# Kernel optimization log

Measured on AMD Instinct MI355X. Metric: run time of the kernel, lower is better.

## Reference

```python
import jax, jax.numpy as jnp
import numpy as np

B, T, D, H = 2, 2048, 512, 8
HD = D // H


def _mha(x, Wi, bi, Wo, bo):
    # torch nn.MultiheadAttention with q=k=v=x, eval mode (no dropout), batch-first math
    b, t, d = x.shape
    qkv = x @ Wi.T + bi                      # (b,t,3D)
    q, k, v = jnp.split(qkv, 3, axis=-1)
    q = q.reshape(b, t, H, HD)
    k = k.reshape(b, t, H, HD)
    v = v.reshape(b, t, H, HD)
    scores = jnp.einsum('bqhd,bkhd->bhqk', q, k) / jnp.sqrt(jnp.float32(HD))
    attn = jax.nn.softmax(scores, axis=-1)   # (b,H,t,t)
    out = jnp.einsum('bhqk,bkhd->bqhd', attn, v).reshape(b, t, d) @ Wo.T + bo
    return out, attn.mean(axis=1)            # weights averaged over heads, torch default


def _block_ids(t, c):
    # importance score is the constant c at every position (grad of sum == ones)
    cum = jnp.cumsum(jnp.full((t,), c, dtype=jnp.float32))
    frac = cum % 1.0
    boundary = (frac < jnp.roll(frac, 1)).astype(jnp.int32)
    return jnp.cumsum(boundary)              # ids in [0, max_blocks]


def _merge(x, ids, m):
    # segment-mean over dynamic blocks; block id 0 (pre-first-boundary) is dropped, as in torch loop i=1..max
    xm = jnp.moveaxis(x, 1, 0)               # (t,b,d)
    sums = jax.ops.segment_sum(xm, ids, num_segments=m + 1)[1:]              # (m,b,d)
    counts = jax.ops.segment_sum(jnp.ones(ids.shape[0], jnp.float32), ids, num_segments=m + 1)[1:]
    merged = sums / (counts[:, None, None] + 1e-10)
    return jnp.moveaxis(merged, 0, 1), counts


def setup_inputs():
    key = jax.random.key(0)
    ks = jax.random.split(key, 12)
    s = 0.02
    d = {'x': jax.random.normal(ks[0], (B, T, D), jnp.float32)}
    for i, n in enumerate(['char', 'block', 'glob']):
        d[n + '_Wi'] = jax.random.normal(ks[1 + 3 * i], (3 * D, D), jnp.float32) * s
        d[n + '_bi'] = jnp.zeros((3 * D,), jnp.float32)
        d[n + '_Wo'] = jax.random.normal(ks[2 + 3 * i], (D, D), jnp.float32) * s
        d[n + '_bo'] = jnp.zeros((D,), jnp.float32)
    d['merge_w'] = jax.random.normal(ks[10], (D,), jnp.float32) * 0.01
    d['merge_b'] = jnp.array([0.37], jnp.float32)
    d['gmerge_w'] = jax.random.normal(ks[11], (D,), jnp.float32) * 0.01
    d['gmerge_b'] = jnp.array([0.41], jnp.float32)
    return d


def reference(x, char_Wi, char_bi, char_Wo, char_bo, block_Wi, block_bi, block_Wo, block_bo,
              glob_Wi, glob_bi, glob_Wo, glob_bo, merge_w, merge_b, gmerge_w, gmerge_b):
    char_out, char_w = _mha(x, char_Wi, char_bi, char_Wo, char_bo)
    c1 = merge_w.sum() + merge_b[0]
    ids1 = _block_ids(T, c1)
    m1 = int(ids1.max())                      # data-independent given weights; concrete in eager
    blocks, cnt1 = _merge(char_out, ids1, m1)
    block_out, block_w = _mha(blocks, block_Wi, block_bi, block_Wo, block_bo)
    c2 = gmerge_w.sum() + gmerge_b[0]
    ids2 = _block_ids(m1, c2)
    m2 = int(ids2.max())
    glob, cnt2 = _merge(block_out, ids2, m2)
    glob_out, glob_w = _mha(glob, glob_Wi, glob_bi, glob_Wo, glob_bo)
    # double repeat_interleave expansion == gather: token t -> char block -> global block
    ids1n = np.asarray(ids1)
    ids2n = np.asarray(ids2)
    token_g = np.where(ids1n >= 1, ids2n[np.maximum(ids1n - 1, 0)], 0)
    tok_idx = np.nonzero(token_g >= 1)[0]
    expanded = glob_out[:, jnp.asarray(token_g[tok_idx] - 1), :]
    return expanded, char_w, block_w, glob_w
```

## Files before the change

### kernel.cpp

```cpp
#include <hip/hip_runtime.h>
#include <cstdint>
#include <cstddef>


#define TB 2
#define TT 2048
#define TD 512
#define TH 8
#define THD 64
#define KC 4

#define MI_M1 0
#define MI_M2 1
#define MI_NTOK 2
#define MI_OFF_CW 3
#define MI_OFF_BW 4
#define MI_OFF_GW 5
#define MI_MCHAR 6
#define MI_MBLOCK 7
#define MI_MGLOB 8
#define MI_SEQC 9
#define MI_SEQB 10
#define MI_SEQG 11

typedef _Float16 half8 __attribute__((ext_vector_type(8)));
typedef _Float16 half4 __attribute__((ext_vector_type(4)));
typedef _Float16 half2_t __attribute__((ext_vector_type(2)));
typedef float floatx4 __attribute__((ext_vector_type(4)));

__device__ __forceinline__ floatx4 mfma16(half8 a, half8 b, floatx4 c) {
  return __builtin_amdgcn_mfma_f32_16x16x32_f16(a, b, c, 0, 0, 0);
}
__device__ __forceinline__ floatx4 mfma16k16(half4 a, half4 b, floatx4 c) {
  return __builtin_amdgcn_mfma_f32_16x16x16f16(a, b, c, 0, 0, 0);
}

__device__ __forceinline__ double fracd(double x) { return x - floor(x); }

__device__ int scan_phase(int n, double c, int* __restrict__ ids,
                          int* __restrict__ startg, float* __restrict__ cntg,
                          int* __restrict__ wsum, int t)
{
  int loc[8];
  const int base = t * 8;
#pragma unroll
  for (int j = 0; j < 8; ++j) {
    const int i = base + j;
    int f = 0;
    if (i < n) {
      const int pidx = (i == 0) ? n : i;
      f = (fracd((double)(i + 1) * c) < fracd((double)pidx * c)) ? 1 : 0;
    }
    loc[j] = f + ((j > 0) ? loc[j - 1] : 0);
  }
  wsum[t] = loc[7];
  __syncthreads();
  for (int off = 1; off < 256; off <<= 1) {
    int u = 0;
    if (t >= off) u = wsum[t - off];
    __syncthreads();
    wsum[t] += u;
    __syncthreads();
  }
  const int excl = wsum[t] - loc[7];
  const int m = wsum[255];
#pragma unroll
  for (int j = 0; j < 8; ++j) {
    const int i = base + j;
    if (i < n) {
      const int id = excl + loc[j];
      ids[i] = id;
      const int f = loc[j] - ((j > 0) ? loc[j - 1] : 0);
      if (f) startg[id - 1] = i;
    }
  }
  __syncthreads();
  for (int j = t; j < m; j += 256)
    cntg[j] = (float)((((j + 1) < m) ? startg[j + 1] : n) - startg[j]);
  __syncthreads();
  return m;
}

__global__ __launch_bounds__(256)
void meta_kernel(const float* __restrict__ mw, const float* __restrict__ mb,
                 const float* __restrict__ gw, const float* __restrict__ gb,
                 int* __restrict__ mi,
                 int* __restrict__ start1, float* __restrict__ cnt1,
                 int* __restrict__ start2, float* __restrict__ cnt2,
                 int* __restrict__ gmap)
{
  __shared__ int ids1[TT];
  __shared__ int ids2[TT];
  __shared__ int wsum[256];
  __shared__ double dsh[256];
  const int t = threadIdx.x;

  double s1 = 0.0, s2 = 0.0;
  for (int i = t; i < TD; i += 256) { s1 += (double)mw[i]; s2 += (double)gw[i]; }
  dsh[t] = s1; __syncthreads();
  for (int off = 128; off > 0; off >>= 1) {
    if (t < off) dsh[t] += dsh[t + off];
    __syncthreads();
  }
  const double c1 = dsh[0] + (double)mb[0];
  __syncthreads();
  dsh[t] = s2; __syncthreads();
  for (int off = 128; off > 0; off >>= 1) {
    if (t < off) dsh[t] += dsh[t + off];
    __syncthreads();
  }
  const double c2 = dsh[0] + (double)gb[0];
  __syncthreads();

  const int m1 = scan_phase(TT, c1, ids1, start1, cnt1, wsum, t);
  const int m2 = scan_phase(m1, c2, ids2, start2, cnt2, wsum, t);

  int i0 = TT;
  if (m1 >= 1 && m2 >= 1) i0 = start1[start2[0]];
  const int ntok = TT - i0;

  if (t == 0) {
    mi[MI_M1] = m1; mi[MI_M2] = m2; mi[MI_NTOK] = ntok;
    const int offcw = TB * ntok * TD;
    mi[MI_OFF_CW] = offcw;
    mi[MI_OFF_BW] = offcw + TB * TT * TT;
    mi[MI_OFF_GW] = offcw + TB * TT * TT + TB * m1 * m1;
    mi[MI_MCHAR] = TB * TT;
    mi[MI_MBLOCK] = TB * m1;
    mi[MI_MGLOB] = TB * m2;
    mi[MI_SEQC] = TT;
    mi[MI_SEQB] = m1;
    mi[MI_SEQG] = m2;
  }
  for (int i = i0 + t; i < TT; i += 256)
    gmap[i - i0] = ids2[ids1[i] - 1] - 1;
}

template <typename OutT, bool SPLIT>
__global__ __launch_bounds__(256)
void gemm_mfma(const float* __restrict__ A, const float* __restrict__ W,
               const float* __restrict__ bias, OutT* __restrict__ C,
               const int* __restrict__ mi, int m_slot, int N)
{
  const int M = mi[m_slot];
  const int bm = blockIdx.y * 128;
  if (bm >= M) return;
  const int bn = blockIdx.x * 64;
  __shared__ _Float16 Ah[128][40];
  __shared__ _Float16 Wh[64][40];
  __shared__ _Float16 Al[SPLIT ? 128 : 1][40];
  __shared__ _Float16 Wl[SPLIT ? 64 : 1][40];

  const int t = threadIdx.x;
  const int wv = t >> 6;
  const int lane = t & 63;
  const int l15 = lane & 15;
  const int quad = lane >> 4;
  const int srowA = t >> 1;
  const int ssegA = (t & 1) * 16;
  const int srowW = t >> 2;
  const int ssegW = (t & 3) * 8;

  floatx4 acc[2][4];
#pragma unroll
  for (int i = 0; i < 2; ++i)
#pragma unroll
    for (int j = 0; j < 4; ++j) acc[i][j] = (floatx4){0.f, 0.f, 0.f, 0.f};

  for (int kk = 0; kk < TD; kk += 32) {
    __syncthreads();
    {
      const int ar = bm + srowA;
#pragma unroll
      for (int u = 0; u < 4; ++u) {
        float4 av = make_float4(0.f, 0.f, 0.f, 0.f);
        if (ar < M) av = *(const float4*)&A[(size_t)ar * TD + kk + ssegA + u * 4];
        const float aa[4] = {av.x, av.y, av.z, av.w};
        half4 hi, lo;
#pragma unroll
        for (int e = 0; e < 4; ++e) {
          const _Float16 h = (_Float16)aa[e];
          hi[e] = h;
          if constexpr (SPLIT) lo[e] = (_Float16)(aa[e] - (float)h);
        }
        *(half4*)&Ah[srowA][ssegA + u * 4] = hi;
        if constexpr (SPLIT) *(half4*)&Al[srowA][ssegA + u * 4] = lo;
      }
#pragma unroll
      for (int u = 0; u < 2; ++u) {
        const float4 wvv = *(const float4*)&W[(size_t)(bn + srowW) * TD + kk + ssegW + u * 4];
        const float ww[4] = {wvv.x, wvv.y, wvv.z, wvv.w};
        half4 hi, lo;
#pragma unroll
        for (int e = 0; e < 4; ++e) {
          const _Float16 h = (_Float16)ww[e];
          hi[e] = h;
          if constexpr (SPLIT) lo[e] = (_Float16)(ww[e] - (float)h);
        }
        *(half4*)&Wh[srowW][ssegW + u * 4] = hi;
        if constexpr (SPLIT) *(half4*)&Wl[srowW][ssegW + u * 4] = lo;
      }
    }
    __syncthreads();
    half8 ah[2], al[2];
#pragma unroll
    for (int mp = 0; mp < 2; ++mp) {
      ah[mp] = *(const half8*)&Ah[wv * 32 + mp * 16 + l15][quad * 8];
      if constexpr (SPLIT) al[mp] = *(const half8*)&Al[wv * 32 + mp * 16 + l15][quad * 8];
    }
#pragma unroll
    for (int np = 0; np < 4; ++np) {
      const half8 bh = *(const half8*)&Wh[np * 16 + l15][quad * 8];
      if constexpr (SPLIT) {
        const half8 bl = *(const half8*)&Wl[np * 16 + l15][quad * 8];
#pragma unroll
        for (int mp = 0; mp < 2; ++mp) {
          acc[mp][np] = mfma16(al[mp], bh, acc[mp][np]);
          acc[mp][np] = mfma16(ah[mp], bl, acc[mp][np]);
          acc[mp][np] = mfma16(ah[mp], bh, acc[mp][np]);
        }
      } else {
#pragma unroll
        for (int mp = 0; mp < 2; ++mp)
          acc[mp][np] = mfma16(ah[mp], bh, acc[mp][np]);
      }
    }
  }
  float bv[4];
#pragma unroll
  for (int np = 0; np < 4; ++np) bv[np] = bias[bn + np * 16 + l15];
#pragma unroll
  for (int mp = 0; mp < 2; ++mp) {
#pragma unroll
    for (int r = 0; r < 4; ++r) {
      const int row = bm + wv * 32 + mp * 16 + quad * 4 + r;
      if (row < M) {
        OutT* cp = &C[(size_t)row * N + bn];
#pragma unroll
        for (int np = 0; np < 4; ++np)
          cp[np * 16 + l15] = (OutT)(acc[mp][np][r] + bv[np]);
      }
    }
  }
}

__global__ __launch_bounds__(256)
void gemm_norm_mfma(const _Float16* __restrict__ Ob, const float* __restrict__ lb,
                    const float* __restrict__ W, const float* __restrict__ bias,
                    float* __restrict__ C, const int* __restrict__ mi,
                    int m_slot, int seq_slot)
{
  const int M = mi[m_slot];
  const int bm = blockIdx.y * 64;
  if (bm >= M) return;
  const int seq = mi[seq_slot];
  const int bn = blockIdx.x * 64;
  __shared__ _Float16 Ah[64][40];
  __shared__ _Float16 Al[64][40];
  __shared__ _Float16 Wh[64][40];
  __shared__ _Float16 Wl[64][40];

  const int t = threadIdx.x;
  const int wv = t >> 6;
  const int lane = t & 63;
  const int l15 = lane & 15;
  const int quad = lane >> 4;
  const int srow = t >> 2;
  const int sseg = (t & 3) * 8;

  const int ar = bm + srow;
  const int ab = (ar >= seq) ? 1 : 0;
  const int aq = ar - ab * seq;

  floatx4 acc[4];
#pragma unroll
  for (int j = 0; j < 4; ++j) acc[j] = (floatx4){0.f, 0.f, 0.f, 0.f};

  for (int kk = 0; kk < TD; kk += 32) {
    __syncthreads();
    {
      float aa[8] = {0.f, 0.f, 0.f, 0.f, 0.f, 0.f, 0.f, 0.f};
      if (ar < M) {
        const size_t off = (size_t)ar * TD + kk + sseg;
#pragma unroll
        for (int z = 0; z < KC; ++z) {
          const half8 hv = *(const half8*)&Ob[(size_t)z * 2097152 + off];
#pragma unroll
          for (int e = 0; e < 8; ++e) aa[e] += (float)hv[e];
        }
        const int h = kk >> 6;
        const size_t lidx = ((size_t)(ab * TH + h)) * 2048 + aq;
        float lt = 0.f;
#pragma unroll
        for (int z = 0; z < KC; ++z) lt += lb[(size_t)z * 32768 + lidx];
        const float linv = 1.f / lt;
#pragma unroll
        for (int e = 0; e < 8; ++e) aa[e] *= linv;
      }
      half8 hi, lo;
#pragma unroll
      for (int e = 0; e < 8; ++e) {
        const _Float16 h = (_Float16)aa[e];
        hi[e] = h; lo[e] = (_Float16)(aa[e] - (float)h);
      }
      *(half8*)&Ah[srow][sseg] = hi;
      *(half8*)&Al[srow][sseg] = lo;

      const float4 w0 = *(const float4*)&W[(size_t)(bn + srow) * TD + kk + sseg];
      const float4 w1 = *(const float4*)&W[(size_t)(bn + srow) * TD + kk + sseg + 4];
      const float ww[8] = {w0.x, w0.y, w0.z, w0.w, w1.x, w1.y, w1.z, w1.w};
      half8 whi, wlo;
#pragma unroll
      for (int e = 0; e < 8; ++e) {
        const _Float16 h = (_Float16)ww[e];
        whi[e] = h; wlo[e] = (_Float16)(ww[e] - (float)h);
      }
      *(half8*)&Wh[srow][sseg] = whi;
      *(half8*)&Wl[srow][sseg] = wlo;
    }
    __syncthreads();
    const half8 ah = *(const half8*)&Ah[wv * 16 + l15][quad * 8];
    const half8 al = *(const half8*)&Al[wv * 16 + l15][quad * 8];
#pragma unroll
    for (int np = 0; np < 4; ++np) {
      const half8 bh = *(const half8*)&Wh[np * 16 + l15][quad * 8];
      const half8 bl = *(const half8*)&Wl[np * 16 + l15][quad * 8];
      acc[np] = mfma16(al, bh, acc[np]);
      acc[np] = mfma16(ah, bl, acc[np]);
      acc[np] = mfma16(ah, bh, acc[np]);
    }
  }
  float bv[4];
#pragma unroll
  for (int np = 0; np < 4; ++np) bv[np] = bias[bn + np * 16 + l15];
#pragma unroll
  for (int r = 0; r < 4; ++r) {
    const int row = bm + wv * 16 + quad * 4 + r;
    if (row < M) {
      float* cp = &C[(size_t)row * 512 + bn];
#pragma unroll
      for (int np = 0; np < 4; ++np)
        cp[np * 16 + l15] = acc[np][r] + bv[np];
    }
  }
}

__global__ __launch_bounds__(256)
void attn1_mfma(const _Float16* __restrict__ qkv,
                float* __restrict__ lbase, _Float16* __restrict__ Obase,
                const int* __restrict__ mi, int seq_slot)
{
  const int seq = mi[seq_slot];
  const int q0 = blockIdx.x * 128;
  if (q0 >= seq) return;
  const int b = blockIdx.y >> 3, h = blockIdx.y & 7;
  const int z = blockIdx.z;
  float* lP = lbase + (size_t)z * 32768;
  _Float16* oP = Obase + (size_t)z * 2097152;
  const int t = threadIdx.x;
  const int wv = t >> 6;
  const int lane = t & 63;
  const int l15 = lane & 15;
  const int quad = lane >> 4;

  __shared__ __align__(16) char smem_raw[18432];
  _Float16 (*Kf)[72] = (_Float16 (*)[72])smem_raw;
  _Float16 (*Vt)[72] = (_Float16 (*)[72])(smem_raw + 9216);
  float    (*Ot)[68] = (float (*)[68])smem_raw;

  half8 qB[2][2];
#pragma unroll
  for (int mp = 0; mp < 2; ++mp) {
    const int qrow = q0 + wv * 32 + mp * 16 + l15;
#pragma unroll
    for (int c = 0; c < 2; ++c) {
      half8 v = {};
      if (qrow < seq)
        v = *(const half8*)&qkv[((size_t)(b * seq + qrow)) * 1536 + h * 64 + c * 32 + quad * 8];
      qB[mp][c] = v;
    }
  }
  half4 onesA;
#pragma unroll
  for (int j = 0; j < 4; ++j) onesA[j] = (_Float16)1.0f;

  floatx4 oacc[2][4];
#pragma unroll
  for (int i = 0; i < 2; ++i)
#pragma unroll
    for (int j = 0; j < 4; ++j) oacc[i][j] = (floatx4){0.f, 0.f, 0.f, 0.f};
  floatx4 lacc[2] = {(floatx4){0.f, 0.f, 0.f, 0.f}, (floatx4){0.f, 0.f, 0.f, 0.f}};

  const int nkt = (seq + 63) >> 6;
  const int nkc = (nkt + KC - 1) / KC;
  const int kt_beg = z * nkc;
  const int kt_end = min(kt_beg + nkc, nkt);

  for (int kt = kt_beg; kt < kt_end; ++kt) {
    const int k0 = kt * 64;
    __syncthreads();
    {
      const int row = t >> 2;
      const int seg = (t & 3) * 16;
      const int kg = k0 + row;
      half8 v0 = {}, v1 = {};
      if (kg < seq) {
        const _Float16* base = &qkv[((size_t)(b * seq + kg)) * 1536 + 512 + h * 64 + seg];
        v0 = *(const half8*)base;
        v1 = *(const half8*)(base + 8);
      }
      *(half8*)&Kf[row][seg] = v0;
      *(half8*)&Kf[row][seg + 8] = v1;
    }
    {
      const int tp = lane & 31;
      const int dsel = lane >> 5;
      const int dbase = wv * 16 + dsel * 8;
      const int kg0 = k0 + tp * 2;
      half8 vA = {}, vB = {};
      if (kg0 < seq)
        vA = *(const half8*)&qkv[((size_t)(b * seq + kg0)) * 1536 + 1024 + h * 64 + dbase];
      if (kg0 + 1 < seq)
        vB = *(const half8*)&qkv[((size_t)(b * seq + kg0 + 1)) * 1536 + 1024 + h * 64 + dbase];
#pragma unroll
      for (int j = 0; j < 8; ++j) {
        half2_t pk; pk[0] = vA[j]; pk[1] = vB[j];
        *(half2_t*)&Vt[dbase + j][tp * 2] = pk;
      }
    }
    __syncthreads();

#pragma unroll
    for (int p = 0; p < 4; ++p) {
      floatx4 sT[2] = {(floatx4){0.f, 0.f, 0.f, 0.f}, (floatx4){0.f, 0.f, 0.f, 0.f}};
#pragma unroll
      for (int c = 0; c < 2; ++c) {
        const half8 kA = *(const half8*)&Kf[p * 16 + l15][c * 32 + quad * 8];
#pragma unroll
        for (int mp = 0; mp < 2; ++mp)
          sT[mp] = mfma16(kA, qB[mp][c], sT[mp]);
      }
      half4 vA[4];
#pragma unroll
      for (int dblk = 0; dblk < 4; ++dblk)
        vA[dblk] = *(const half4*)&Vt[dblk * 16 + l15][p * 16 + quad * 4];
      const int kg = k0 + p * 16 + quad * 4;
#pragma unroll
      for (int mp = 0; mp < 2; ++mp) {
        half4 eB;
#pragma unroll
        for (int r = 0; r < 4; ++r) {
          const float e = (kg + r < seq) ? __expf(sT[mp][r] * 0.125f) : 0.f;
          eB[r] = (_Float16)e;
        }
        lacc[mp] = mfma16k16(onesA, eB, lacc[mp]);
#pragma unroll
        for (int dblk = 0; dblk < 4; ++dblk)
          oacc[mp][dblk] = mfma16k16(vA[dblk], eB, oacc[mp][dblk]);
      }
    }
  }

  __syncthreads();

#pragma unroll
  for (int mp = 0; mp < 2; ++mp) {
#pragma unroll
    for (int dblk = 0; dblk < 4; ++dblk)
      *(floatx4*)&Ot[wv * 16 + l15][dblk * 16 + quad * 4] = oacc[mp][dblk];
    const int ql = lane >> 2;
    const int dseg = (lane & 3) * 4;
    const int qg = q0 + wv * 32 + mp * 16 + ql;
    if (qg < seq) {
      _Float16* op = &oP[((size_t)(b * seq + qg)) * 512 + h * 64];
#pragma unroll
      for (int u = 0; u < 4; ++u) {
        const float4 v = *(const float4*)&Ot[wv * 16 + ql][u * 16 + dseg];
        half4 hv;
        hv[0] = (_Float16)v.x; hv[1] = (_Float16)v.y;
        hv[2] = (_Float16)v.z; hv[3] = (_Float16)v.w;
        *(half4*)(op + u * 16 + dseg) = hv;
      }
    }
    if (quad == 0) {
      const int qg2 = q0 + wv * 32 + mp * 16 + l15;
      if (qg2 < seq)
        lP[((size_t)(b * TH + h)) * 2048 + qg2] = lacc[mp][0];
    }
  }
}

__global__ __launch_bounds__(256)
void attn2_mfma(const _Float16* __restrict__ qkv,
                const float* __restrict__ lb,
                float* __restrict__ outb, const int* __restrict__ mi,
                int seq_slot, int off_slot)
{
  const int seq = mi[seq_slot];
  const int q0 = blockIdx.y * 64;
  const int k0 = blockIdx.x * 128;
  if (q0 >= seq || k0 >= seq) return;
  const int b = blockIdx.z;
  const int woff = mi[off_slot];
  float* wout = outb + (size_t)woff + (size_t)b * seq * seq;

  __shared__ _Float16 Qs[64][72];
  __shared__ _Float16 Ksh[128][72];
  __shared__ float Linv[64];

  const int t = threadIdx.x;
  const int wv = t >> 6;
  const int lane = t & 63;
  const int l15 = lane & 15;
  const int quad = lane >> 4;
  const int srowQ = t >> 2;
  const int ssegQ = (t & 3) * 16;
  const int srowK = t >> 1;
  const int ssegK = (t & 1) * 32;

  floatx4 acc[8];
#pragma unroll
  for (int j = 0; j < 8; ++j) acc[j] = (floatx4){0.f, 0.f, 0.f, 0.f};

  for (int h = 0; h < TH; ++h) {
    __syncthreads();
    {
      const int qr = q0 + srowQ;
      half8 q0v = {}, q1v = {};
      if (qr < seq) {
        const _Float16* base = &qkv[((size_t)(b * seq + qr)) * 1536 + h * 64 + ssegQ];
        q0v = *(const half8*)base;
        q1v = *(const half8*)(base + 8);
      }
      *(half8*)&Qs[srowQ][ssegQ] = q0v;
      *(half8*)&Qs[srowQ][ssegQ + 8] = q1v;

      const int kr = k0 + srowK;
#pragma unroll
      for (int u = 0; u < 4; ++u) {
        half8 kv = {};
        if (kr < seq)
          kv = *(const half8*)&qkv[((size_t)(b * seq + kr)) * 1536 + 512 + h * 64 + ssegK + u * 8];
        *(half8*)&Ksh[srowK][ssegK + u * 8] = kv;
      }
      if (t < 64) {
        float lv = 1.f;
        if (q0 + t < seq) {
          const size_t lidx = ((size_t)(b * TH + h)) * 2048 + q0 + t;
          float lt = 0.f;
#pragma unroll
          for (int z = 0; z < KC; ++z) lt += lb[(size_t)z * 32768 + lidx];
          lv = lt;
        }
        Linv[t] = 1.f / lv;
      }
    }
    __syncthreads();

    half8 af[2];
#pragma unroll
    for (int c = 0; c < 2; ++c)
      af[c] = *(const half8*)&Qs[wv * 16 + l15][c * 32 + quad * 8];
    float lv[4];
#pragma unroll
    for (int r = 0; r < 4; ++r)
      lv[r] = Linv[wv * 16 + quad * 4 + r];

#pragma unroll
    for (int np = 0; np < 8; ++np) {
      half8 bf[2];
#pragma unroll
      for (int c = 0; c < 2; ++c)
        bf[c] = *(const half8*)&Ksh[np * 16 + l15][c * 32 + quad * 8];
      floatx4 s = (floatx4){0.f, 0.f, 0.f, 0.f};
      s = mfma16(af[0], bf[0], s);
      s = mfma16(af[1], bf[1], s);
#pragma unroll
      for (int r = 0; r < 4; ++r)
        acc[np][r] += __expf(s[r] * 0.125f) * lv[r];
    }
  }

#pragma unroll
  for (int r = 0; r < 4; ++r) {
    const int qg = q0 + wv * 16 + quad * 4 + r;
    if (qg >= seq) continue;
    float* rowp = wout + (size_t)qg * seq;
#pragma unroll
    for (int np = 0; np < 8; ++np) {
      const int col = k0 + np * 16 + l15;
      if (col < seq) rowp[col] = acc[np][r] * 0.125f;
    }
  }
}

__global__ __launch_bounds__(256)
void merge_kernel(const float* __restrict__ src, float* __restrict__ dst,
                  const int* __restrict__ start, const float* __restrict__ cnt,
                  const int* __restrict__ mi, int seqin_slot, int seqout_slot)
{
  const int j = blockIdx.x;
  const int b = blockIdx.y;
  const int seqo = mi[seqout_slot];
  if (j >= seqo) return;
  const int seqi = mi[seqin_slot];
  const int s = start[j];
  const float cf = cnt[j];
  const int n = (int)cf;
  const int d0 = threadIdx.x * 2;
  float s0 = 0.f, s1 = 0.f;
  const float* p = &src[((size_t)b * seqi + s) * TD + d0];
  for (int i = 0; i < n; ++i) {
    const float2 v = *(const float2*)p;
    s0 += v.x; s1 += v.y;
    p += TD;
  }
  const float inv = 1.f / (cf + 1e-10f);
  float2 o; o.x = s0 * inv; o.y = s1 * inv;
  *(float2*)&dst[((size_t)b * seqo + j) * TD + d0] = o;
}

__global__ __launch_bounds__(256)
void expand_kernel(const float* __restrict__ gout, float* __restrict__ dout,
                   const int* __restrict__ gmap, const int* __restrict__ mi)
{
  const int j = blockIdx.x;
  const int b = blockIdx.y;
  const int ntok = mi[MI_NTOK];
  if (j >= ntok) return;
  const int m2 = mi[MI_M2];
  const int g = gmap[j];
  const int d0 = threadIdx.x * 2;
  const float2 v = *(const float2*)&gout[((size_t)b * m2 + g) * TD + d0];
  *(float2*)&dout[((size_t)b * ntok + j) * TD + d0] = v;
}

extern "C" void kernel_launch(void* const* d_in, const int* in_sizes, int n_in,
                              void* d_out, int out_size, void* d_ws, size_t ws_size,
                              hipStream_t stream)
{
  const float* x   = (const float*)d_in[0];
  const float* cWi = (const float*)d_in[1];
  const float* cbi = (const float*)d_in[2];
  const float* cWo = (const float*)d_in[3];
  const float* cbo = (const float*)d_in[4];
  const float* bWi = (const float*)d_in[5];
  const float* bbi = (const float*)d_in[6];
  const float* bWo = (const float*)d_in[7];
  const float* bbo = (const float*)d_in[8];
  const float* gWi = (const float*)d_in[9];
  const float* gbi = (const float*)d_in[10];
  const float* gWo = (const float*)d_in[11];
  const float* gbo = (const float*)d_in[12];
  const float* mw  = (const float*)d_in[13];
  const float* mbv = (const float*)d_in[14];
  const float* gw  = (const float*)d_in[15];
  const float* gbv = (const float*)d_in[16];
  float* outf = (float*)d_out;

  char* wsb = (char*)d_ws;
  int*   mi     = (int*)(wsb);
  int*   start1 = (int*)(wsb + 1024);
  float* cnt1   = (float*)(wsb + 1024 + 8192);
  int*   start2 = (int*)(wsb + 1024 + 2 * 8192);
  float* cnt2   = (float*)(wsb + 1024 + 3 * 8192);
  int*   gmap   = (int*)(wsb + 1024 + 4 * 8192);
  float* lbase  = (float*)(wsb + 65536);
  _Float16* qkv = (_Float16*)(wsb + 655360);
  _Float16* Obase = (_Float16*)(wsb + 655360 + 12582912);
  float* stg_o  = (float*)(wsb + 655360 + 12582912 + (size_t)KC * 4194304);
  float* stg_m  = stg_o + 2097152;

  const dim3 blk(256);

  meta_kernel<<<dim3(1), blk, 0, stream>>>(mw, mbv, gw, gbv, mi, start1, cnt1, start2, cnt2, gmap);

  gemm_mfma<_Float16, false><<<dim3(24, 32), blk, 0, stream>>>(x, cWi, cbi, qkv, mi, MI_MCHAR, 1536);
  attn1_mfma<<<dim3(16, 16, KC), blk, 0, stream>>>(qkv, lbase, Obase, mi, MI_SEQC);
  attn2_mfma<<<dim3(16, 32, 2), blk, 0, stream>>>(qkv, lbase, outf, mi, MI_SEQC, MI_OFF_CW);
  gemm_norm_mfma<<<dim3(8, 64), blk, 0, stream>>>(Obase, lbase, cWo, cbo, stg_o, mi, MI_MCHAR, MI_SEQC);
  merge_kernel<<<dim3(2048, 2), blk, 0, stream>>>(stg_o, stg_m, start1, cnt1, mi, MI_SEQC, MI_SEQB);

  gemm_mfma<_Float16, false><<<dim3(24, 32), blk, 0, stream>>>(stg_m, bWi, bbi, qkv, mi, MI_MBLOCK, 1536);
  attn1_mfma<<<dim3(16, 16, KC), blk, 0, stream>>>(qkv, lbase, Obase, mi, MI_SEQB);
  attn2_mfma<<<dim3(16, 32, 2), blk, 0, stream>>>(qkv, lbase, outf, mi, MI_SEQB, MI_OFF_BW);
  gemm_norm_mfma<<<dim3(8, 64), blk, 0, stream>>>(Obase, lbase, bWo, bbo, stg_o, mi, MI_MBLOCK, MI_SEQB);
  merge_kernel<<<dim3(2048, 2), blk, 0, stream>>>(stg_o, stg_m, start2, cnt2, mi, MI_SEQB, MI_SEQG);

  gemm_mfma<_Float16, false><<<dim3(24, 32), blk, 0, stream>>>(stg_m, gWi, gbi, qkv, mi, MI_MGLOB, 1536);
  attn1_mfma<<<dim3(16, 16, KC), blk, 0, stream>>>(qkv, lbase, Obase, mi, MI_SEQG);
  attn2_mfma<<<dim3(16, 32, 2), blk, 0, stream>>>(qkv, lbase, outf, mi, MI_SEQG, MI_OFF_GW);
  gemm_norm_mfma<<<dim3(8, 64), blk, 0, stream>>>(Obase, lbase, gWo, gbo, stg_o, mi, MI_MGLOB, MI_SEQG);
  expand_kernel<<<dim3(2048, 2), blk, 0, stream>>>(stg_o, outf, gmap, mi);

  (void)in_sizes; (void)n_in; (void)out_size; (void)ws_size;
}
```

Baseline: 398.4 us.

## Enlarge attention-weight tile to 128 queries and use exp2 with folded scale

The head-averaged attention-weight kernel now handles 128 query rows per block instead of 64. Each wave computes two 16-row sub-tiles that share the loaded K fragments, and the grid is halved, so K tiles are reloaded from global memory half as often. The exponentials in both attention kernels switch from __expf with a 0.125 scale to exp2f with the scale and log2(e) folded into one constant. The first attention kernel also skips the per-element bounds check on full key tiles. The larger tile doubles accumulator registers and shared memory per block, which may reduce occupancy, and halves the number of blocks.

```diff
diff --git a/kernel.cpp b/kernel.cpp
--- a/kernel.cpp
+++ b/kernel.cpp
@@ -23,6 +23,8 @@
 #define MI_SEQB 10
 #define MI_SEQG 11
 
+#define CEXP 0.1803368801111244f
+
 typedef _Float16 half8 __attribute__((ext_vector_type(8)));
 typedef _Float16 half4 __attribute__((ext_vector_type(4)));
 typedef _Float16 half2_t __attribute__((ext_vector_type(2)));
@@ -398,6 +400,7 @@
 
   for (int kt = kt_beg; kt < kt_end; ++kt) {
     const int k0 = kt * 64;
+    const bool full = (k0 + 64 <= seq);
     __syncthreads();
     {
       const int row = t >> 2;
@@ -448,10 +451,16 @@
 #pragma unroll
       for (int mp = 0; mp < 2; ++mp) {
         half4 eB;
-#pragma unroll
-        for (int r = 0; r < 4; ++r) {
-          const float e = (kg + r < seq) ? __expf(sT[mp][r] * 0.125f) : 0.f;
-          eB[r] = (_Float16)e;
+        if (full) {
+#pragma unroll
+          for (int r = 0; r < 4; ++r)
+            eB[r] = (_Float16)exp2f(sT[mp][r] * CEXP);
+        } else {
+#pragma unroll
+          for (int r = 0; r < 4; ++r) {
+            const float e = (kg + r < seq) ? exp2f(sT[mp][r] * CEXP) : 0.f;
+            eB[r] = (_Float16)e;
+          }
         }
         lacc[mp] = mfma16k16(onesA, eB, lacc[mp]);
 #pragma unroll
@@ -497,53 +506,47 @@
                 int seq_slot, int off_slot)
 {
   const int seq = mi[seq_slot];
-  const int q0 = blockIdx.y * 64;
+  const int q0 = blockIdx.y * 128;
   const int k0 = blockIdx.x * 128;
   if (q0 >= seq || k0 >= seq) return;
   const int b = blockIdx.z;
   const int woff = mi[off_slot];
   float* wout = outb + (size_t)woff + (size_t)b * seq * seq;
 
-  __shared__ _Float16 Qs[64][72];
+  __shared__ _Float16 Qs[128][72];
   __shared__ _Float16 Ksh[128][72];
-  __shared__ float Linv[64];
+  __shared__ float Linv[128];
 
   const int t = threadIdx.x;
   const int wv = t >> 6;
   const int lane = t & 63;
   const int l15 = lane & 15;
   const int quad = lane >> 4;
-  const int srowQ = t >> 2;
-  const int ssegQ = (t & 3) * 16;
-  const int srowK = t >> 1;
-  const int ssegK = (t & 1) * 32;
-
-  floatx4 acc[8];
-#pragma unroll
-  for (int j = 0; j < 8; ++j) acc[j] = (floatx4){0.f, 0.f, 0.f, 0.f};
+  const int srow = t >> 1;
+  const int sseg = (t & 1) * 32;
+
+  floatx4 acc[2][8];
+#pragma unroll
+  for (int i = 0; i < 2; ++i)
+#pragma unroll
+    for (int j = 0; j < 8; ++j) acc[i][j] = (floatx4){0.f, 0.f, 0.f, 0.f};
 
   for (int h = 0; h < TH; ++h) {
     __syncthreads();
     {
-      const int qr = q0 + srowQ;
-      half8 q0v = {}, q1v = {};
-      if (qr < seq) {
-        const _Float16* base = &qkv[((size_t)(b * seq + qr)) * 1536 + h * 64 + ssegQ];
-        q0v = *(const half8*)base;
-        q1v = *(const half8*)(base + 8);
-      }
-      *(half8*)&Qs[srowQ][ssegQ] = q0v;
-      *(half8*)&Qs[srowQ][ssegQ + 8] = q1v;
-
-      const int kr = k0 + srowK;
+      const int qr = q0 + srow;
+      const int kr = k0 + srow;
 #pragma unroll
       for (int u = 0; u < 4; ++u) {
-        half8 kv = {};
+        half8 qv = {}, kv = {};
+        if (qr < seq)
+          qv = *(const half8*)&qkv[((size_t)(b * seq + qr)) * 1536 + h * 64 + sseg + u * 8];
         if (kr < seq)
-          kv = *(const half8*)&qkv[((size_t)(b * seq + kr)) * 1536 + 512 + h * 64 + ssegK + u * 8];
-        *(half8*)&Ksh[srowK][ssegK + u * 8] = kv;
-      }
-      if (t < 64) {
+          kv = *(const half8*)&qkv[((size_t)(b * seq + kr)) * 1536 + 512 + h * 64 + sseg + u * 8];
+        *(half8*)&Qs[srow][sseg + u * 8] = qv;
+        *(half8*)&Ksh[srow][sseg + u * 8] = kv;
+      }
+      if (t < 128) {
         float lv = 1.f;
         if (q0 + t < seq) {
           const size_t lidx = ((size_t)(b * TH + h)) * 2048 + q0 + t;
@@ -557,14 +560,18 @@
     }
     __syncthreads();
 
-    half8 af[2];
-#pragma unroll
-    for (int c = 0; c < 2; ++c)
-      af[c] = *(const half8*)&Qs[wv * 16 + l15][c * 32 + quad * 8];
-    float lv[4];
-#pragma unroll
-    for (int r = 0; r < 4; ++r)
-      lv[r] = Linv[wv * 16 + quad * 4 + r];
+    half8 af[2][2];
+#pragma unroll
+    for (int mp = 0; mp < 2; ++mp)
+#pragma unroll
+      for (int c = 0; c < 2; ++c)
+        af[mp][c] = *(const half8*)&Qs[wv * 32 + mp * 16 + l15][c * 32 + quad * 8];
+    float lv[2][4];
+#pragma unroll
+    for (int mp = 0; mp < 2; ++mp)
+#pragma unroll
+      for (int r = 0; r < 4; ++r)
+        lv[mp][r] = Linv[wv * 32 + mp * 16 + quad * 4 + r];
 
 #pragma unroll
     for (int np = 0; np < 8; ++np) {
@@ -572,24 +579,30 @@
 #pragma unroll
       for (int c = 0; c < 2; ++c)
         bf[c] = *(const half8*)&Ksh[np * 16 + l15][c * 32 + quad * 8];
-      floatx4 s = (floatx4){0.f, 0.f, 0.f, 0.f};
-      s = mfma16(af[0], bf[0], s);
-      s = mfma16(af[1], bf[1], s);
-#pragma unroll
-      for (int r = 0; r < 4; ++r)
-        acc[np][r] += __expf(s[r] * 0.125f) * lv[r];
-    }
-  }
-
-#pragma unroll
-  for (int r = 0; r < 4; ++r) {
-    const int qg = q0 + wv * 16 + quad * 4 + r;
-    if (qg >= seq) continue;
-    float* rowp = wout + (size_t)qg * seq;
-#pragma unroll
-    for (int np = 0; np < 8; ++np) {
-      const int col = k0 + np * 16 + l15;
-      if (col < seq) rowp[col] = acc[np][r] * 0.125f;
+#pragma unroll
+      for (int mp = 0; mp < 2; ++mp) {
+        floatx4 s = (floatx4){0.f, 0.f, 0.f, 0.f};
+        s = mfma16(af[mp][0], bf[0], s);
+        s = mfma16(af[mp][1], bf[1], s);
+#pragma unroll
+        for (int r = 0; r < 4; ++r)
+          acc[mp][np][r] += exp2f(s[r] * CEXP) * lv[mp][r];
+      }
+    }
+  }
+
+#pragma unroll
+  for (int mp = 0; mp < 2; ++mp) {
+#pragma unroll
+    for (int r = 0; r < 4; ++r) {
+      const int qg = q0 + wv * 32 + mp * 16 + quad * 4 + r;
+      if (qg >= seq) continue;
+      float* rowp = wout + (size_t)qg * seq;
+#pragma unroll
+      for (int np = 0; np < 8; ++np) {
+        const int col = k0 + np * 16 + l15;
+        if (col < seq) rowp[col] = acc[mp][np][r] * 0.125f;
+      }
     }
   }
 }
@@ -677,19 +690,19 @@
 
   gemm_mfma<_Float16, false><<<dim3(24, 32), blk, 0, stream>>>(x, cWi, cbi, qkv, mi, MI_MCHAR, 1536);
   attn1_mfma<<<dim3(16, 16, KC), blk, 0, stream>>>(qkv, lbase, Obase, mi, MI_SEQC);
-  attn2_mfma<<<dim3(16, 32, 2), blk, 0, stream>>>(qkv, lbase, outf, mi, MI_SEQC, MI_OFF_CW);
+  attn2_mfma<<<dim3(16, 16, 2), blk, 0, stream>>>(qkv, lbase, outf, mi, MI_SEQC, MI_OFF_CW);
   gemm_norm_mfma<<<dim3(8, 64), blk, 0, stream>>>(Obase, lbase, cWo, cbo, stg_o, mi, MI_MCHAR, MI_SEQC);
   merge_kernel<<<dim3(2048, 2), blk, 0, stream>>>(stg_o, stg_m, start1, cnt1, mi, MI_SEQC, MI_SEQB);
 
   gemm_mfma<_Float16, false><<<dim3(24, 32), blk, 0, stream>>>(stg_m, bWi, bbi, qkv, mi, MI_MBLOCK, 1536);
   attn1_mfma<<<dim3(16, 16, KC), blk, 0, stream>>>(qkv, lbase, Obase, mi, MI_SEQB);
-  attn2_mfma<<<dim3(16, 32, 2), blk, 0, stream>>>(qkv, lbase, outf, mi, MI_SEQB, MI_OFF_BW);
+  attn2_mfma<<<dim3(16, 16, 2), blk, 0, stream>>>(qkv, lbase, outf, mi, MI_SEQB, MI_OFF_BW);
   gemm_norm_mfma<<<dim3(8, 64), blk, 0, stream>>>(Obase, lbase, bWo, bbo, stg_o, mi, MI_MBLOCK, MI_SEQB);
   merge_kernel<<<dim3(2048, 2), blk, 0, stream>>>(stg_o, stg_m, start2, cnt2, mi, MI_SEQB, MI_SEQG);
 
   gemm_mfma<_Float16, false><<<dim3(24, 32), blk, 0, stream>>>(stg_m, gWi, gbi, qkv, mi, MI_MGLOB, 1536);
   attn1_mfma<<<dim3(16, 16, KC), blk, 0, stream>>>(qkv, lbase, Obase, mi, MI_SEQG);
-  attn2_mfma<<<dim3(16, 32, 2), blk, 0, stream>>>(qkv, lbase, outf, mi, MI_SEQG, MI_OFF_GW);
+  attn2_mfma<<<dim3(16, 16, 2), blk, 0, stream>>>(qkv, lbase, outf, mi, MI_SEQG, MI_OFF_GW);
   gemm_norm_mfma<<<dim3(8, 64), blk, 0, stream>>>(Obase, lbase, gWo, gbo, stg_o, mi, MI_MGLOB, MI_SEQG);
   expand_kernel<<<dim3(2048, 2), blk, 0, stream>>>(stg_o, outf, gmap, mi);
 
```

After: 464.6 us. 16.6% more time.
